# Performance work log

Hardware: AMD Instinct MI355X
Metric: run time of the kernel (lower is better)

## Reference

```python
import jax, jax.numpy as jnp
import numpy as np
from jax import lax

DIM = 512
HEADS = 8
HEAD_DIM = DIM // HEADS
FS = 56            # features_size -> H = W = 56
SR = 2             # sr_ratio
N = FS * FS        # query tokens = 3136
KN = (FS // SR) ** 2  # kv tokens = 784
B = 4
SCALE = HEAD_DIM ** -0.5
LN_EPS = 1e-5


def _relative_indices(fs):
    # matches generate_relative_distance: [[x, y] for x in range(fs) for y in range(fs)]
    coords = np.stack(np.meshgrid(np.arange(fs), np.arange(fs), indexing='ij'), -1).reshape(-1, 2)
    dist = coords[None, :, :] - coords[:, None, :] + (fs - 1)   # (N, N, 2), values in [0, 2fs-2]
    return jnp.asarray(dist, dtype=jnp.int32)


def setup_inputs() -> dict:
    key = jax.random.key(0)
    ks = jax.random.split(key, 8)
    s = 0.02
    return {
        'x':    jax.random.normal(ks[0], (B, DIM, FS, FS), jnp.float32),
        'Wq':   jax.random.normal(ks[1], (DIM, DIM), jnp.float32) * s,
        'Wkv':  jax.random.normal(ks[2], (DIM, 2 * DIM), jnp.float32) * s,
        'Wsr':  jax.random.normal(ks[3], (DIM, DIM, SR, SR), jnp.float32) * s,  # OIHW
        'b_sr': jnp.zeros((DIM,), jnp.float32),
        'gamma': jnp.ones((DIM,), jnp.float32),
        'beta':  jnp.zeros((DIM,), jnp.float32),
        'Wp':   jax.random.normal(ks[4], (DIM, DIM), jnp.float32) * s,
        'bp':   jnp.zeros((DIM,), jnp.float32),
        'pos':  jax.random.normal(ks[5], (2 * FS - 1, 2 * FS - 1), jnp.float32) * 0.2,
        'rel_idx': _relative_indices(FS),
    }


def reference(x, Wq, Wkv, Wsr, b_sr, gamma, beta, Wp, bp, pos, rel_idx):
    b, c, h, w = x.shape
    n = h * w
    xq = x.reshape(b, c, n).transpose(0, 2, 1)                      # B N C
    q = (xq @ Wq).reshape(b, n, HEADS, HEAD_DIM).transpose(0, 2, 1, 3)  # B h N d

    # spatial reduction of k/v: Conv2d(k=SR, s=SR) + LayerNorm
    xr = lax.conv_general_dilated(x, Wsr, (SR, SR), 'VALID',
                                  dimension_numbers=('NCHW', 'OIHW', 'NCHW'))
    xr = xr + b_sr[None, :, None, None]
    kn = xr.shape[2] * xr.shape[3]
    xkv = xr.reshape(b, c, kn).transpose(0, 2, 1)                   # B KN C
    mu = xkv.mean(-1, keepdims=True)
    var = ((xkv - mu) ** 2).mean(-1, keepdims=True)
    xkv = (xkv - mu) * lax.rsqrt(var + LN_EPS) * gamma + beta

    # kv projection; rearrange 'B N (dim h l) -> l B h N dim'
    kv = (xkv @ Wkv).reshape(b, kn, HEAD_DIM, HEADS, 2)
    k = kv[..., 0].transpose(0, 3, 1, 2)                            # B h KN d
    v = kv[..., 1].transpose(0, 3, 1, 2)                            # B h KN d

    attn = jnp.einsum('bhnd,bhmd->bhnm', q, k) * SCALE              # B h N KN
    bias = pos[rel_idx[:, :kn, 0], rel_idx[:, :kn, 1]]              # N KN gathered bias
    attn = jax.nn.softmax(attn + bias, axis=-1)

    out = jnp.einsum('bhnm,bhmd->bhnd', attn, v)                    # B h N d
    out = out.transpose(0, 2, 1, 3).reshape(b, n, c)                # B N C
    out = out @ Wp + bp
    return out.transpose(0, 2, 1).reshape(b, c, h, w)
```

## Files before the change

### kernel.cpp

```cpp
#include <hip/hip_runtime.h>
#include <hip/hip_bf16.h>
#include <cstdint>

constexpr int BATCH = 4;
constexpr int CDIM  = 512;
constexpr int NHEAD = 8;
constexpr int HD    = 64;
constexpr int FSP   = 56;
constexpr int NTOK  = FSP * FSP;
constexpr int KH    = 28;
constexpr int KNTOK = KH * KH;
constexpr float SCALE_ATT = 0.125f;
constexpr int BIAS_LD = 832;

typedef _Float16 f16;
typedef __attribute__((ext_vector_type(8))) _Float16 half8;
typedef __attribute__((ext_vector_type(4))) _Float16 half4;
typedef __attribute__((ext_vector_type(4))) float  floatx4;

__device__ __forceinline__ void tr64(const float* __restrict__ in,
                                     f16* __restrict__ out, int R, int C,
                                     int r0, int c0, float (*sm)[65], int tid) {
  const int rr = tid >> 2, cs = (tid & 3) * 16;
  const float* src = in + (size_t)(r0 + rr) * C + c0 + cs;
#pragma unroll
  for (int j = 0; j < 16; j += 4) *(float4*)&sm[rr][cs + j] = *(const float4*)&src[j];
  __syncthreads();
  f16* dh = out + (size_t)(c0 + rr) * R + r0 + cs;
  half8 v0, v1;
#pragma unroll
  for (int j = 0; j < 8; ++j) v0[j] = (f16)sm[cs + j][rr];
#pragma unroll
  for (int j = 0; j < 8; ++j) v1[j] = (f16)sm[cs + 8 + j][rr];
  *(half8*)&dh[0] = v0;
  *(half8*)&dh[8] = v1;
}

__global__ __launch_bounds__(256) void k_prep(const float* __restrict__ x,
                                              const float* __restrict__ Wq,
                                              const float* __restrict__ Wkv,
                                              const float* __restrict__ Wp,
                                              const float* __restrict__ Wsr,
                                              const float* __restrict__ pos,
                                              f16* __restrict__ xT,
                                              f16* __restrict__ WqT,
                                              f16* __restrict__ WkvT,
                                              f16* __restrict__ WpT,
                                              f16* __restrict__ WsrP,
                                              f16* __restrict__ biasT) {
  __shared__ float sm[64][65];
  const int tid = threadIdx.x;
  int bid = blockIdx.x;
  if (bid < 1568) {
    const int b = bid / 392, r = bid % 392;
    tr64(x + (size_t)b * CDIM * NTOK, xT + (size_t)b * NTOK * CDIM,
         CDIM, NTOK, (r % 8) * 64, (r / 8) * 64, sm, tid);
    return;
  }
  bid -= 1568;
  if (bid < 64)  { tr64(Wq,  WqT,  512, 512,  (bid % 8) * 64, (bid / 8) * 64, sm, tid); return; }
  bid -= 64;
  if (bid < 128) { tr64(Wkv, WkvT, 512, 1024, (bid % 8) * 64, (bid / 8) * 64, sm, tid); return; }
  bid -= 128;
  if (bid < 64)  { tr64(Wp,  WpT,  512, 512,  (bid % 8) * 64, (bid / 8) * 64, sm, tid); return; }
  bid -= 64;
  if (bid < 512) {
    const float* src = Wsr + (size_t)bid * 2048;
    f16* dh = WsrP + (size_t)bid * 2048;
    for (int kp = tid; kp < 2048; kp += 256) {
      const int dd = kp >> 9, c = kp & 511;
      dh[kp] = (f16)src[c * 4 + dd];
    }
    return;
  }
  bid -= 512;
  {
    const int n = bid;
    const int in_ = n / FSP, jn = n % FSP;
    const int cbase = 55 * 111 + 55 - in_ * 111 - jn;
    for (int i = tid; i < BIAS_LD; i += 256) {
      const int jc = i >> 6, w = i & 63, txx = w >> 2, tt = w & 3;
      const int m = jc * 64 + tt * 16 + txx;
      float v = -30000.f;
      if (m < KNTOK) {
        const int im = m / FSP, jm = m % FSP;
        v = pos[cbase + im * 111 + jm];
      }
      biasT[(size_t)n * BIAS_LD + i] = (f16)v;
    }
  }
}

struct GemmSmem { f16 A[3][128 * 32]; f16 B[3][128 * 32]; };

__device__ __forceinline__ void gl_lds(const f16* g, f16* l) {
  __builtin_amdgcn_global_load_lds(
      (const __attribute__((address_space(1))) void*)g,
      (__attribute__((address_space(3))) void*)l, 16, 0, 0);
}

__device__ __forceinline__ void gemm128(GemmSmem* sm,
    const f16* a0, const f16* a1, const f16* b0, const f16* b1,
    int lane, int wv, int wm, int wn, int quad, int tx,
    floatx4 acc[4][4]) {
  const int so = wv * 1024 + lane * 8;
  gl_lds(a0,      &sm->A[0][so]);
  gl_lds(a1,      &sm->A[0][so + 512]);
  gl_lds(b0,      &sm->B[0][so]);
  gl_lds(b1,      &sm->B[0][so + 512]);
  gl_lds(a0 + 32, &sm->A[1][so]);
  gl_lds(a1 + 32, &sm->A[1][so + 512]);
  gl_lds(b0 + 32, &sm->B[1][so]);
  gl_lds(b1 + 32, &sm->B[1][so + 512]);
  asm volatile("s_waitcnt vmcnt(4)" ::: "memory");
  __builtin_amdgcn_s_barrier();
#pragma unroll
  for (int it = 0; it < 16; ++it) {
    const int cur = it % 3;
    if (it < 14) {
      const int pf = (it + 2) % 3;
      gl_lds(a0 + (it + 2) * 32, &sm->A[pf][so]);
      gl_lds(a1 + (it + 2) * 32, &sm->A[pf][so + 512]);
      gl_lds(b0 + (it + 2) * 32, &sm->B[pf][so]);
      gl_lds(b1 + (it + 2) * 32, &sm->B[pf][so + 512]);
    }
    half8 af[4], bf[4];
#pragma unroll
    for (int i = 0; i < 4; ++i)
      af[i] = *(const half8*)&sm->A[cur][(wm * 64 + i * 16 + tx) * 32 + quad * 8];
#pragma unroll
    for (int j = 0; j < 4; ++j)
      bf[j] = *(const half8*)&sm->B[cur][(wn * 64 + j * 16 + tx) * 32 + quad * 8];
#pragma unroll
    for (int j = 0; j < 4; ++j)
#pragma unroll
      for (int i = 0; i < 4; ++i)
        acc[i][j] = __builtin_amdgcn_mfma_f32_16x16x32_f16(af[i], bf[j], acc[i][j], 0, 0, 0);
    __builtin_amdgcn_sched_barrier(0);
    if (it < 14) asm volatile("s_waitcnt vmcnt(4)" ::: "memory");
    else         asm volatile("s_waitcnt vmcnt(0)" ::: "memory");
    __builtin_amdgcn_s_barrier();
  }
}

#define GEMM128_PRE()                                                     \
  const int tid = threadIdx.x, lane = tid & 63, wv = tid >> 6;            \
  const int wm = wv & 1, wn = wv >> 1, quad = lane >> 4, tx = lane & 15;  \
  const int lr = lane >> 2, lc = (lane & 3) * 8;                          \
  floatx4 acc[4][4];                                                      \
  _Pragma("unroll") for (int i = 0; i < 4; ++i)                           \
  _Pragma("unroll") for (int j = 0; j < 4; ++j)                           \
      acc[i][j] = (floatx4){0.f, 0.f, 0.f, 0.f};

__global__ __launch_bounds__(256) void k_gemmA(const f16* __restrict__ xT,
                                               const f16* __restrict__ WqT,
                                               f16* __restrict__ Qh,
                                               const f16* __restrict__ WsrP,
                                               float* __restrict__ XRp) {
  __shared__ GemmSmem sm;
  GEMM128_PRE();
  int bid = blockIdx.x;
  if (bid < 400) {
    const int b = bid / 100, t = bid % 100;
    const int m0 = (t >> 2) * 128, n0 = (t & 3) * 128;
    const f16* xb = xT + (size_t)b * NTOK * CDIM;
    const int r0 = wv * 32 + lr, r1 = r0 + 16;
    const f16* a0 = xb + (size_t)min(m0 + r0, NTOK - 1) * CDIM + lc;
    const f16* a1 = xb + (size_t)min(m0 + r1, NTOK - 1) * CDIM + lc;
    const f16* b0 = WqT + (size_t)(n0 + r0) * CDIM + lc;
    const f16* b1 = WqT + (size_t)(n0 + r1) * CDIM + lc;
    gemm128(&sm, a0, a1, b0, b1, lane, wv, wm, wn, quad, tx, acc);
    f16* qhB = Qh + (size_t)b * NTOK * CDIM;
#pragma unroll
    for (int i = 0; i < 4; ++i)
#pragma unroll
      for (int rg = 0; rg < 4; ++rg) {
        const int m = m0 + wm * 64 + i * 16 + quad * 4 + rg;
        if (m >= NTOK) continue;
#pragma unroll
        for (int j = 0; j < 4; ++j)
          qhB[(size_t)m * CDIM + n0 + wn * 64 + j * 16 + tx] = (f16)acc[i][j][rg];
      }
  } else {
    bid -= 400;
    const int bkc = bid / 28, r = bid % 28;
    const int b = bkc >> 2, kc = bkc & 3;
    const int m0 = (r >> 2) * 128, n0 = (r & 3) * 128;
    const f16* xb = xT + (size_t)b * NTOK * CDIM;
    const int r0 = wv * 32 + lr, r1 = r0 + 16;
    int am0 = m0 + r0; if (am0 >= KNTOK) am0 = 0;
    int am1 = m0 + r1; if (am1 >= KNTOK) am1 = 0;
    const int sp0 = 112 * (am0 / KH) + 2 * (am0 % KH) + (kc >> 1) * FSP + (kc & 1);
    const int sp1 = 112 * (am1 / KH) + 2 * (am1 % KH) + (kc >> 1) * FSP + (kc & 1);
    const f16* a0 = xb + (size_t)sp0 * CDIM + lc;
    const f16* a1 = xb + (size_t)sp1 * CDIM + lc;
    const f16* b0 = WsrP + (size_t)(n0 + r0) * 2048 + kc * 512 + lc;
    const f16* b1 = WsrP + (size_t)(n0 + r1) * 2048 + kc * 512 + lc;
    gemm128(&sm, a0, a1, b0, b1, lane, wv, wm, wn, quad, tx, acc);
    float* dst = XRp + (size_t)(kc * BATCH + b) * KNTOK * CDIM;
#pragma unroll
    for (int i = 0; i < 4; ++i)
#pragma unroll
      for (int rg = 0; rg < 4; ++rg) {
        const int m = m0 + wm * 64 + i * 16 + quad * 4 + rg;
        if (m >= KNTOK) continue;
#pragma unroll
        for (int j = 0; j < 4; ++j)
          dst[(size_t)m * CDIM + n0 + wn * 64 + j * 16 + tx] = acc[i][j][rg];
      }
  }
}

__global__ __launch_bounds__(256) void k_ln(const float* __restrict__ XRp,
                                            const float* __restrict__ b_sr,
                                            const float* __restrict__ gamma,
                                            const float* __restrict__ beta,
                                            f16* __restrict__ oh) {
  const int row = blockIdx.x;
  const size_t slab = (size_t)BATCH * KNTOK * CDIM;
  const float* p = XRp + (size_t)row * CDIM;
  const int tid = threadIdx.x;
  const float v0 = p[tid] + p[tid + slab] + p[tid + 2 * slab] + p[tid + 3 * slab]
                 + b_sr[tid];
  const float v1 = p[tid + 256] + p[tid + 256 + slab] + p[tid + 256 + 2 * slab]
                 + p[tid + 256 + 3 * slab] + b_sr[tid + 256];
  float s = v0 + v1;
  float s2 = v0 * v0 + v1 * v1;
#pragma unroll
  for (int mask = 32; mask >= 1; mask >>= 1) {
    s  += __shfl_xor(s, mask, 64);
    s2 += __shfl_xor(s2, mask, 64);
  }
  __shared__ float ws[4], ws2[4];
  const int wid = tid >> 6;
  if ((tid & 63) == 0) { ws[wid] = s; ws2[wid] = s2; }
  __syncthreads();
  const float ts  = ws[0] + ws[1] + ws[2] + ws[3];
  const float ts2 = ws2[0] + ws2[1] + ws2[2] + ws2[3];
  const float mu  = ts * (1.f / CDIM);
  const float var = ts2 * (1.f / CDIM) - mu * mu;
  const float rs  = rsqrtf(var + 1e-5f);
  const size_t base = (size_t)row * CDIM;
  oh[base + tid]       = (f16)((v0 - mu) * rs * gamma[tid] + beta[tid]);
  oh[base + tid + 256] = (f16)((v1 - mu) * rs * gamma[tid + 256] + beta[tid + 256]);
}

__global__ __launch_bounds__(256) void k_kvproj(const f16* __restrict__ XRh,
                                                const f16* __restrict__ WkvT,
                                                f16* __restrict__ Kh,
                                                f16* __restrict__ Vt) {
  __shared__ GemmSmem sm;
  GEMM128_PRE();
  const int bid = blockIdx.x;
  const int b = bid / 56, r = bid % 56;
  const int m0 = (r / 8) * 128, n0 = (r % 8) * 128;
  const f16* ab = XRh + (size_t)b * KNTOK * CDIM;
  const int r0 = wv * 32 + lr, r1 = r0 + 16;
  const f16* a0 = ab + (size_t)min(m0 + r0, KNTOK - 1) * CDIM + lc;
  const f16* a1 = ab + (size_t)min(m0 + r1, KNTOK - 1) * CDIM + lc;
  const f16* b0 = WkvT + (size_t)(n0 + r0) * CDIM + lc;
  const f16* b1 = WkvT + (size_t)(n0 + r1) * CDIM + lc;
  gemm128(&sm, a0, a1, b0, b1, lane, wv, wm, wn, quad, tx, acc);
#pragma unroll
  for (int i = 0; i < 4; ++i)
#pragma unroll
    for (int rg = 0; rg < 4; ++rg) {
      const int m = m0 + wm * 64 + i * 16 + quad * 4 + rg;
      if (m >= KNTOK) continue;
#pragma unroll
      for (int j = 0; j < 4; ++j) {
        const int o2 = n0 + wn * 64 + j * 16 + tx;
        const int d = o2 >> 4, hh = (o2 >> 1) & 7;
        const float v = acc[i][j][rg];
        if (o2 & 1)
          Vt[((size_t)(b * NHEAD + hh) * HD + d) * KNTOK + m] = (f16)v;
        else
          Kh[((size_t)(b * NHEAD + hh) * KNTOK + m) * HD + d] = (f16)v;
      }
    }
}

#define LSTR 72
__global__ __launch_bounds__(256) void k_attn(const f16* __restrict__ Qh,
                                              const f16* __restrict__ Kh,
                                              const f16* __restrict__ Vt,
                                              const f16* __restrict__ biasT,
                                              f16* __restrict__ Oh) {
  __shared__ f16 Qhs[128][LSTR];
  __shared__ f16 Khs[2][64][LSTR], Vts[2][64][LSTR];
  __shared__ f16 Ps[4][32][LSTR];
  const int b = blockIdx.x >> 3, h = blockIdx.x & 7;
  const int n0 = blockIdx.y * 128;
  const int tid = threadIdx.x, lane = tid & 63, wv = tid >> 6;
  const int quad = lane >> 4, tx = lane & 15;
  const int rr = tid >> 2, sg = (tid & 3) * 16;
  const int qr = tid >> 1, qs = (tid & 1) * 32;

  const f16* khB = Kh + (size_t)(b * NHEAD + h) * KNTOK * HD;
  const f16* vtB = Vt + (size_t)(b * NHEAD + h) * HD * KNTOK;

  {
    const int qrow = min(n0 + qr, NTOK - 1);
    const f16* src = Qh + ((size_t)b * NTOK + qrow) * CDIM + h * HD + qs;
    *(half8*)&Qhs[qr][qs]      = *(const half8*)&src[0];
    *(half8*)&Qhs[qr][qs + 8]  = *(const half8*)&src[8];
    *(half8*)&Qhs[qr][qs + 16] = *(const half8*)&src[16];
    *(half8*)&Qhs[qr][qs + 24] = *(const half8*)&src[24];
    const size_t koff = (size_t)rr * HD + sg;
    *(half8*)&Khs[0][rr][sg]     = *(const half8*)&khB[koff];
    *(half8*)&Khs[0][rr][sg + 8] = *(const half8*)&khB[koff + 8];
    const size_t voff = (size_t)rr * KNTOK + sg;
    *(half8*)&Vts[0][rr][sg]     = *(const half8*)&vtB[voff];
    *(half8*)&Vts[0][rr][sg + 8] = *(const half8*)&vtB[voff + 8];
  }

  size_t bbase[2][4];
#pragma unroll
  for (int i = 0; i < 2; ++i)
#pragma unroll
    for (int rg = 0; rg < 4; ++rg) {
      const int grow = min(n0 + wv * 32 + i * 16 + quad * 4 + rg, NTOK - 1);
      bbase[i][rg] = (size_t)grow * BIAS_LD + tx * 4;
    }

  floatx4 acc_o[2][4];
#pragma unroll
  for (int i = 0; i < 2; ++i)
#pragma unroll
    for (int t = 0; t < 4; ++t) acc_o[i][t] = (floatx4){0.f, 0.f, 0.f, 0.f};
  float l_part[2][4] = {};
  __syncthreads();

  half8 nk0, nk1, nv0, nv1;
  for (int jc = 0; jc < 13; ++jc) {
    const int cur = jc & 1, nxt = cur ^ 1;
    if (jc < 12) {
      const int mbn = (jc + 1) * 64;
      const int km = min(mbn + rr, KNTOK - 1);
      const size_t koff = (size_t)km * HD + sg;
      nk0 = *(const half8*)&khB[koff];
      nk1 = *(const half8*)&khB[koff + 8];
      const int vc = min(mbn + sg, KNTOK - 16);
      const size_t voff = (size_t)rr * KNTOK + vc;
      nv0 = *(const half8*)&vtB[voff];
      nv1 = *(const half8*)&vtB[voff + 8];
    }

    floatx4 sc[2][4];
#pragma unroll
    for (int i = 0; i < 2; ++i)
#pragma unroll
      for (int t = 0; t < 4; ++t) sc[i][t] = (floatx4){0.f, 0.f, 0.f, 0.f};
#pragma unroll
    for (int ks = 0; ks < 2; ++ks) {
      const int kk = ks * 32 + quad * 8;
      half8 aq[2];
#pragma unroll
      for (int i = 0; i < 2; ++i)
        aq[i] = *(const half8*)&Qhs[wv * 32 + i * 16 + tx][kk];
#pragma unroll
      for (int t = 0; t < 4; ++t) {
        const half8 bk = *(const half8*)&Khs[cur][t * 16 + tx][kk];
#pragma unroll
        for (int i = 0; i < 2; ++i)
          sc[i][t] = __builtin_amdgcn_mfma_f32_16x16x32_f16(aq[i], bk, sc[i][t], 0, 0, 0);
      }
    }

#pragma unroll
    for (int i = 0; i < 2; ++i)
#pragma unroll
      for (int rg = 0; rg < 4; ++rg) {
        const half4 bb = *(const half4*)&biasT[bbase[i][rg] + jc * 64];
        const float p0 = __expf(fmaf(sc[i][0][rg], SCALE_ATT, (float)bb[0]));
        const float p1 = __expf(fmaf(sc[i][1][rg], SCALE_ATT, (float)bb[1]));
        const float p2 = __expf(fmaf(sc[i][2][rg], SCALE_ATT, (float)bb[2]));
        const float p3 = __expf(fmaf(sc[i][3][rg], SCALE_ATT, (float)bb[3]));
        l_part[i][rg] += (p0 + p1) + (p2 + p3);
        const int prow = i * 16 + quad * 4 + rg;
        Ps[wv][prow][0 * 16 + tx] = (f16)p0;
        Ps[wv][prow][1 * 16 + tx] = (f16)p1;
        Ps[wv][prow][2 * 16 + tx] = (f16)p2;
        Ps[wv][prow][3 * 16 + tx] = (f16)p3;
      }

#pragma unroll
    for (int ks = 0; ks < 2; ++ks) {
      const int kk = ks * 32 + quad * 8;
      half8 ap[2];
#pragma unroll
      for (int i = 0; i < 2; ++i)
        ap[i] = *(const half8*)&Ps[wv][i * 16 + tx][kk];
#pragma unroll
      for (int t = 0; t < 4; ++t) {
        const half8 bv = *(const half8*)&Vts[cur][t * 16 + tx][kk];
#pragma unroll
        for (int i = 0; i < 2; ++i)
          acc_o[i][t] = __builtin_amdgcn_mfma_f32_16x16x32_f16(ap[i], bv, acc_o[i][t], 0, 0, 0);
      }
    }
    if (jc < 12) {
      *(half8*)&Khs[nxt][rr][sg]     = nk0;
      *(half8*)&Khs[nxt][rr][sg + 8] = nk1;
      *(half8*)&Vts[nxt][rr][sg]     = nv0;
      *(half8*)&Vts[nxt][rr][sg + 8] = nv1;
    }
    __syncthreads();
  }

#pragma unroll
  for (int i = 0; i < 2; ++i)
#pragma unroll
    for (int rg = 0; rg < 4; ++rg) {
      float l = l_part[i][rg];
#pragma unroll
      for (int msk = 1; msk < 16; msk <<= 1) l += __shfl_xor(l, msk, 64);
      const float inv = 1.f / l;
      const int grow = n0 + wv * 32 + i * 16 + quad * 4 + rg;
      if (grow < NTOK) {
        const size_t base = ((size_t)b * NTOK + grow) * CDIM + h * HD;
#pragma unroll
        for (int t = 0; t < 4; ++t)
          Oh[base + t * 16 + tx] = (f16)(acc_o[i][t][rg] * inv);
      }
    }
}

__global__ __launch_bounds__(256) void k_outproj(const f16* __restrict__ Og,
                                                 const f16* __restrict__ WpT,
                                                 const float* __restrict__ bp,
                                                 float* __restrict__ out) {
  __shared__ GemmSmem sm;
  GEMM128_PRE();
  const int bid = blockIdx.x;
  const int b = bid / 100, t = bid % 100;
  const int m0 = (t >> 2) * 128, n0 = (t & 3) * 128;
  const f16* ab = Og + (size_t)b * NTOK * CDIM;
  const int r0 = wv * 32 + lr, r1 = r0 + 16;
  const f16* a0 = ab + (size_t)min(m0 + r0, NTOK - 1) * CDIM + lc;
  const f16* a1 = ab + (size_t)min(m0 + r1, NTOK - 1) * CDIM + lc;
  const f16* b0 = WpT + (size_t)(n0 + r0) * CDIM + lc;
  const f16* b1 = WpT + (size_t)(n0 + r1) * CDIM + lc;
  gemm128(&sm, a0, a1, b0, b1, lane, wv, wm, wn, quad, tx, acc);
#pragma unroll
  for (int j = 0; j < 4; ++j) {
    const int co = n0 + wn * 64 + j * 16 + tx;
    const float bpv = bp[co];
    float* obase = out + ((size_t)b * CDIM + co) * NTOK;
#pragma unroll
    for (int i = 0; i < 4; ++i) {
      const int mb4 = m0 + wm * 64 + i * 16 + quad * 4;
      if (mb4 < NTOK) {
        floatx4 v = acc[i][j] + bpv;
        *(floatx4*)&obase[mb4] = v;
      }
    }
  }
}

extern "C" void kernel_launch(void* const* d_in, const int* in_sizes, int n_in,
                              void* d_out, int out_size, void* d_ws, size_t ws_size,
                              hipStream_t stream) {
  const float* x     = (const float*)d_in[0];
  const float* Wq    = (const float*)d_in[1];
  const float* Wkv   = (const float*)d_in[2];
  const float* Wsr   = (const float*)d_in[3];
  const float* b_sr  = (const float*)d_in[4];
  const float* gamma = (const float*)d_in[5];
  const float* beta  = (const float*)d_in[6];
  const float* Wp    = (const float*)d_in[7];
  const float* bp    = (const float*)d_in[8];
  const float* pos   = (const float*)d_in[9];
  float* out = (float*)d_out;

  char* p = (char*)d_ws;
  auto alloc = [&](size_t bytes) -> void* {
    void* r = (void*)p;
    p += (bytes + 255) & ~(size_t)255;
    return r;
  };
  const size_t SZ_BNC = (size_t)BATCH * NTOK * CDIM;
  const size_t SZ_BKC = (size_t)BATCH * KNTOK * CDIM;
  const size_t SZ_KV  = (size_t)BATCH * NHEAD * KNTOK * HD;

  f16* xT    = (f16*)alloc(SZ_BNC * 2);
  f16* WqT   = (f16*)alloc(512 * 512 * 2);
  f16* WkvT  = (f16*)alloc(1024 * 512 * 2);
  f16* WpT   = (f16*)alloc(512 * 512 * 2);
  f16* WsrP  = (f16*)alloc(512 * 2048 * 2);
  f16* Qh    = (f16*)alloc(SZ_BNC * 2);
  float* XRp = (float*)alloc(SZ_BKC * 4 * 4);
  f16* XRh   = (f16*)alloc(SZ_BKC * 2);
  f16* Vt    = (f16*)alloc(SZ_KV * 2);
  f16* biasT = (f16*)alloc((size_t)NTOK * BIAS_LD * 2);

  f16* Kh = (f16*)XRp;
  f16* Og = xT;

  const dim3 blk(256);
  k_prep   <<<dim3(5472), blk, 0, stream>>>(x, Wq, Wkv, Wp, Wsr, pos,
                                            xT, WqT, WkvT, WpT, WsrP, biasT);
  k_gemmA  <<<dim3(848),  blk, 0, stream>>>(xT, WqT, Qh, WsrP, XRp);
  k_ln     <<<dim3(BATCH * KNTOK), blk, 0, stream>>>(XRp, b_sr, gamma, beta, XRh);
  k_kvproj <<<dim3(224),  blk, 0, stream>>>(XRh, WkvT, Kh, Vt);
  k_attn   <<<dim3(BATCH * NHEAD, 25), blk, 0, stream>>>(Qh, Kh, Vt, biasT, Og);
  k_outproj<<<dim3(400),  blk, 0, stream>>>(Og, WpT, bp, out);
}
```

Baseline: 273.8 us.

## Transpose score MFMA, linearize bias layout, and use one wave per LayerNorm row

The attention kernel swaps the MFMA operand order so each lane holds four consecutive key columns of one query row. This lets the bias be read with contiguous half4 loads from a simple linear layout and lets P be written to LDS as packed half2 pairs. It also makes the row-sum reduction need only two cross-lane shuffles, and Q fragments are hoisted out of the key loop into registers. The LayerNorm kernel now processes one row per wavefront with float4 loads and half8 stores, dropping the shared-memory reduction and block barrier, at the cost of more registers for the hoisted Q.

```diff
diff --git a/kernel.cpp b/kernel.cpp
--- a/kernel.cpp
+++ b/kernel.cpp
@@ -16,6 +16,7 @@
 typedef _Float16 f16;
 typedef __attribute__((ext_vector_type(8))) _Float16 half8;
 typedef __attribute__((ext_vector_type(4))) _Float16 half4;
+typedef __attribute__((ext_vector_type(2))) _Float16 half2v;
 typedef __attribute__((ext_vector_type(4))) float  floatx4;
 
 __device__ __forceinline__ void tr64(const float* __restrict__ in,
@@ -79,8 +80,7 @@
     const int in_ = n / FSP, jn = n % FSP;
     const int cbase = 55 * 111 + 55 - in_ * 111 - jn;
     for (int i = tid; i < BIAS_LD; i += 256) {
-      const int jc = i >> 6, w = i & 63, txx = w >> 2, tt = w & 3;
-      const int m = jc * 64 + tt * 16 + txx;
+      const int m = i;
       float v = -30000.f;
       if (m < KNTOK) {
         const int im = m / FSP, jm = m % FSP;
@@ -216,33 +216,39 @@
                                             const float* __restrict__ gamma,
                                             const float* __restrict__ beta,
                                             f16* __restrict__ oh) {
-  const int row = blockIdx.x;
+  const int tid = threadIdx.x, wv = tid >> 6, lane = tid & 63;
+  const int row = blockIdx.x * 4 + wv;
   const size_t slab = (size_t)BATCH * KNTOK * CDIM;
-  const float* p = XRp + (size_t)row * CDIM;
-  const int tid = threadIdx.x;
-  const float v0 = p[tid] + p[tid + slab] + p[tid + 2 * slab] + p[tid + 3 * slab]
-                 + b_sr[tid];
-  const float v1 = p[tid + 256] + p[tid + 256 + slab] + p[tid + 256 + 2 * slab]
-                 + p[tid + 256 + 3 * slab] + b_sr[tid + 256];
-  float s = v0 + v1;
-  float s2 = v0 * v0 + v1 * v1;
+  const float* p = XRp + (size_t)row * CDIM + lane * 8;
+  float v[8];
+#pragma unroll
+  for (int j = 0; j < 8; j += 4) {
+    float4 a0 = *(const float4*)&p[j];
+    float4 a1 = *(const float4*)&p[j + slab];
+    float4 a2 = *(const float4*)&p[j + 2 * slab];
+    float4 a3 = *(const float4*)&p[j + 3 * slab];
+    float4 bs = *(const float4*)&b_sr[lane * 8 + j];
+    v[j]     = a0.x + a1.x + a2.x + a3.x + bs.x;
+    v[j + 1] = a0.y + a1.y + a2.y + a3.y + bs.y;
+    v[j + 2] = a0.z + a1.z + a2.z + a3.z + bs.z;
+    v[j + 3] = a0.w + a1.w + a2.w + a3.w + bs.w;
+  }
+  float s = 0.f, s2 = 0.f;
+#pragma unroll
+  for (int j = 0; j < 8; ++j) { s += v[j]; s2 += v[j] * v[j]; }
 #pragma unroll
   for (int mask = 32; mask >= 1; mask >>= 1) {
     s  += __shfl_xor(s, mask, 64);
     s2 += __shfl_xor(s2, mask, 64);
   }
-  __shared__ float ws[4], ws2[4];
-  const int wid = tid >> 6;
-  if ((tid & 63) == 0) { ws[wid] = s; ws2[wid] = s2; }
-  __syncthreads();
-  const float ts  = ws[0] + ws[1] + ws[2] + ws[3];
-  const float ts2 = ws2[0] + ws2[1] + ws2[2] + ws2[3];
-  const float mu  = ts * (1.f / CDIM);
-  const float var = ts2 * (1.f / CDIM) - mu * mu;
+  const float mu  = s * (1.f / CDIM);
+  const float var = s2 * (1.f / CDIM) - mu * mu;
   const float rs  = rsqrtf(var + 1e-5f);
-  const size_t base = (size_t)row * CDIM;
-  oh[base + tid]       = (f16)((v0 - mu) * rs * gamma[tid] + beta[tid]);
-  oh[base + tid + 256] = (f16)((v1 - mu) * rs * gamma[tid + 256] + beta[tid + 256]);
+  half8 o;
+#pragma unroll
+  for (int j = 0; j < 8; ++j)
+    o[j] = (f16)((v[j] - mu) * rs * gamma[lane * 8 + j] + beta[lane * 8 + j]);
+  *(half8*)&oh[(size_t)row * CDIM + lane * 8] = o;
 }
 
 __global__ __launch_bounds__(256) void k_kvproj(const f16* __restrict__ XRh,
@@ -314,22 +320,27 @@
     *(half8*)&Vts[0][rr][sg + 8] = *(const half8*)&vtB[voff + 8];
   }
 
-  size_t bbase[2][4];
+  size_t bbase[2];
+#pragma unroll
+  for (int i = 0; i < 2; ++i) {
+    const int grow = min(n0 + wv * 32 + i * 16 + tx, NTOK - 1);
+    bbase[i] = (size_t)grow * BIAS_LD + quad * 4;
+  }
+
+  floatx4 acc_o[2][4];
 #pragma unroll
   for (int i = 0; i < 2; ++i)
 #pragma unroll
-    for (int rg = 0; rg < 4; ++rg) {
-      const int grow = min(n0 + wv * 32 + i * 16 + quad * 4 + rg, NTOK - 1);
-      bbase[i][rg] = (size_t)grow * BIAS_LD + tx * 4;
-    }
-
-  floatx4 acc_o[2][4];
+    for (int t = 0; t < 4; ++t) acc_o[i][t] = (floatx4){0.f, 0.f, 0.f, 0.f};
+  float l_part[2] = {0.f, 0.f};
+  __syncthreads();
+
+  half8 aq[2][2];
 #pragma unroll
   for (int i = 0; i < 2; ++i)
 #pragma unroll
-    for (int t = 0; t < 4; ++t) acc_o[i][t] = (floatx4){0.f, 0.f, 0.f, 0.f};
-  float l_part[2][4] = {};
-  __syncthreads();
+    for (int ks = 0; ks < 2; ++ks)
+      aq[i][ks] = *(const half8*)&Qhs[wv * 32 + i * 16 + tx][ks * 32 + quad * 8];
 
   half8 nk0, nk1, nv0, nv1;
   for (int jc = 0; jc < 13; ++jc) {
@@ -354,35 +365,32 @@
 #pragma unroll
     for (int ks = 0; ks < 2; ++ks) {
       const int kk = ks * 32 + quad * 8;
-      half8 aq[2];
-#pragma unroll
-      for (int i = 0; i < 2; ++i)
-        aq[i] = *(const half8*)&Qhs[wv * 32 + i * 16 + tx][kk];
 #pragma unroll
       for (int t = 0; t < 4; ++t) {
         const half8 bk = *(const half8*)&Khs[cur][t * 16 + tx][kk];
 #pragma unroll
         for (int i = 0; i < 2; ++i)
-          sc[i][t] = __builtin_amdgcn_mfma_f32_16x16x32_f16(aq[i], bk, sc[i][t], 0, 0, 0);
-      }
-    }
-
-#pragma unroll
-    for (int i = 0; i < 2; ++i)
-#pragma unroll
-      for (int rg = 0; rg < 4; ++rg) {
-        const half4 bb = *(const half4*)&biasT[bbase[i][rg] + jc * 64];
-        const float p0 = __expf(fmaf(sc[i][0][rg], SCALE_ATT, (float)bb[0]));
-        const float p1 = __expf(fmaf(sc[i][1][rg], SCALE_ATT, (float)bb[1]));
-        const float p2 = __expf(fmaf(sc[i][2][rg], SCALE_ATT, (float)bb[2]));
-        const float p3 = __expf(fmaf(sc[i][3][rg], SCALE_ATT, (float)bb[3]));
-        l_part[i][rg] += (p0 + p1) + (p2 + p3);
-        const int prow = i * 16 + quad * 4 + rg;
-        Ps[wv][prow][0 * 16 + tx] = (f16)p0;
-        Ps[wv][prow][1 * 16 + tx] = (f16)p1;
-        Ps[wv][prow][2 * 16 + tx] = (f16)p2;
-        Ps[wv][prow][3 * 16 + tx] = (f16)p3;
-      }
+          sc[i][t] = __builtin_amdgcn_mfma_f32_16x16x32_f16(bk, aq[i][ks], sc[i][t], 0, 0, 0);
+      }
+    }
+
+#pragma unroll
+    for (int i = 0; i < 2; ++i) {
+      const int prow = i * 16 + tx;
+#pragma unroll
+      for (int t = 0; t < 4; ++t) {
+        const half4 bb = *(const half4*)&biasT[bbase[i] + jc * 64 + t * 16];
+        const float p0 = __expf(fmaf(sc[i][t][0], SCALE_ATT, (float)bb[0]));
+        const float p1 = __expf(fmaf(sc[i][t][1], SCALE_ATT, (float)bb[1]));
+        const float p2 = __expf(fmaf(sc[i][t][2], SCALE_ATT, (float)bb[2]));
+        const float p3 = __expf(fmaf(sc[i][t][3], SCALE_ATT, (float)bb[3]));
+        l_part[i] += (p0 + p1) + (p2 + p3);
+        half2v h01 = {(f16)p0, (f16)p1};
+        half2v h23 = {(f16)p2, (f16)p3};
+        *(half2v*)&Ps[wv][prow][t * 16 + quad * 4]     = h01;
+        *(half2v*)&Ps[wv][prow][t * 16 + quad * 4 + 2] = h23;
+      }
+    }
 
 #pragma unroll
     for (int ks = 0; ks < 2; ++ks) {
@@ -409,13 +417,13 @@
   }
 
 #pragma unroll
-  for (int i = 0; i < 2; ++i)
+  for (int i = 0; i < 2; ++i) {
+    float l = l_part[i];
+    l += __shfl_xor(l, 16, 64);
+    l += __shfl_xor(l, 32, 64);
 #pragma unroll
     for (int rg = 0; rg < 4; ++rg) {
-      float l = l_part[i][rg];
-#pragma unroll
-      for (int msk = 1; msk < 16; msk <<= 1) l += __shfl_xor(l, msk, 64);
-      const float inv = 1.f / l;
+      const float inv = 1.f / __shfl(l, quad * 4 + rg, 64);
       const int grow = n0 + wv * 32 + i * 16 + quad * 4 + rg;
       if (grow < NTOK) {
         const size_t base = ((size_t)b * NTOK + grow) * CDIM + h * HD;
@@ -424,6 +432,7 @@
           Oh[base + t * 16 + tx] = (f16)(acc_o[i][t][rg] * inv);
       }
     }
+  }
 }
 
 __global__ __launch_bounds__(256) void k_outproj(const f16* __restrict__ Og,
@@ -501,7 +510,7 @@
   k_prep   <<<dim3(5472), blk, 0, stream>>>(x, Wq, Wkv, Wp, Wsr, pos,
                                             xT, WqT, WkvT, WpT, WsrP, biasT);
   k_gemmA  <<<dim3(848),  blk, 0, stream>>>(xT, WqT, Qh, WsrP, XRp);
-  k_ln     <<<dim3(BATCH * KNTOK), blk, 0, stream>>>(XRp, b_sr, gamma, beta, XRh);
+  k_ln     <<<dim3(BATCH * KNTOK / 4), blk, 0, stream>>>(XRp, b_sr, gamma, beta, XRh);
   k_kvproj <<<dim3(224),  blk, 0, stream>>>(XRh, WkvT, Kh, Vt);
   k_attn   <<<dim3(BATCH * NHEAD, 25), blk, 0, stream>>>(Qh, Kh, Vt, biasT, Og);
   k_outproj<<<dim3(400),  blk, 0, stream>>>(Og, WpT, bp, out);
```

Result: no change. 273.4 us (median of 2 runs) (-0.2%).
